# Kernel tuning notes

Measured on AMD Instinct MI355X. Metric: run time of the kernel, lower is better.

Reference implementation:

```python
import jax, jax.numpy as jnp
import numpy as np

BIN_SIZE = 128
DIST_MULT = 0.1
CLIP_LOW = 0.0
LN_EPS = 1e-6


def setup_inputs() -> dict:
    key = jax.random.key(0)
    ks = jax.random.split(key, 16)
    B, N, F, DD, MAXB = 8, 12800, 256, 128, 200
    s = 0.05  # ~TF random_normal initializer stddev
    inp = {}
    inp["x"] = jax.random.normal(ks[0], (B, N, F), jnp.float32)
    inp["msk"] = jax.random.uniform(ks[1], (B, N)) < 0.9
    # layernorm params
    inp["ln_g"] = jnp.ones((F,), jnp.float32)
    inp["ln_b"] = jnp.zeros((F,), jnp.float32)
    # ffn_dist: Dense(DD, elu) -> Dense(DD)
    inp["w1"] = jax.random.normal(ks[2], (F, DD), jnp.float32) * s
    inp["b1"] = jax.random.normal(ks[3], (DD,), jnp.float32) * s
    inp["w2"] = jax.random.normal(ks[4], (DD, DD), jnp.float32) * s
    inp["b2"] = jax.random.normal(ks[5], (DD,), jnp.float32) * s
    # LSH random rotations (non-trainable)
    inp["rot"] = jax.random.normal(ks[6], (DD, MAXB // 2), jnp.float32) * s
    # two GHConvDense layers (hidden=F -> output=F)
    inp["theta0"] = jax.random.normal(ks[7], (F, F), jnp.float32) * s
    inp["wh0"] = jax.random.normal(ks[8], (F, F), jnp.float32) * s
    inp["wt0"] = jax.random.normal(ks[9], (F, F), jnp.float32) * s
    inp["bt0"] = jax.random.normal(ks[10], (F,), jnp.float32) * s
    inp["theta1"] = jax.random.normal(ks[11], (F, F), jnp.float32) * s
    inp["wh1"] = jax.random.normal(ks[12], (F, F), jnp.float32) * s
    inp["wt1"] = jax.random.normal(ks[13], (F, F), jnp.float32) * s
    inp["bt1"] = jax.random.normal(ks[14], (F,), jnp.float32) * s
    return inp


def _ghconv(x, adj, mskf, theta, wh, wt, bt):
    # x: [B,nb,bs,F], adj: [B,nb,bs,bs], mskf: [B,nb,bs,1]
    deg = jnp.clip(jnp.sum(jnp.abs(adj), axis=-1), 0.0, 1000.0)  # [B,nb,bs]
    norm = ((deg + 1e-6) ** -0.5)[..., None] * mskf
    f_hom = jnp.matmul(x * mskf, theta) * mskf
    f_hom = jnp.matmul(adj, f_hom * norm) * norm
    f_het = jnp.matmul(x * mskf, wh)
    gate = jax.nn.sigmoid(jnp.matmul(x, wt) + bt)
    out = gate * f_hom + (1.0 - gate) * f_het
    return jax.nn.elu(out) * mskf


def _forward(x, msk, ln_g, ln_b, w1, b1, w2, b2, rot,
             theta0, wh0, wt0, bt0, theta1, wh1, wt1, bt1):
    B, N, F = x.shape
    nbins = N // BIN_SIZE
    # layernorm
    mu = jnp.mean(x, axis=-1, keepdims=True)
    var = jnp.mean((x - mu) ** 2, axis=-1, keepdims=True)
    xn = (x - mu) * jax.lax.rsqrt(var + LN_EPS) * ln_g + ln_b
    # ffn_dist
    xd = jnp.matmul(jax.nn.elu(jnp.matmul(xn, w1) + b1), w2) + b2  # [B,N,DD]
    # LSH binning
    mul = jnp.matmul(xd, rot[:, : nbins // 2])
    cmul = jnp.concatenate([mul, -mul], axis=-1)  # [B,N,nbins]
    bin_idx = jnp.argmax(cmul, axis=-1) + jnp.where(~msk, nbins - 1, 0)
    bins_split = jnp.argsort(bin_idx, axis=-1).reshape(B, nbins, BIN_SIZE)
    flat = bins_split.reshape(B, N)
    # gather into bins
    xd_b = jnp.take_along_axis(xd, flat[:, :, None], axis=1).reshape(B, nbins, BIN_SIZE, -1)
    x_b = jnp.take_along_axis(xn, flat[:, :, None], axis=1).reshape(B, nbins, BIN_SIZE, F)
    mskf = msk.astype(x.dtype)[:, :, None]
    m_b = jnp.take_along_axis(mskf, flat[:, :, None], axis=1).reshape(B, nbins, BIN_SIZE, 1)
    # pairwise gaussian kernel within bins
    na = jnp.sum(xd_b * xd_b, axis=-1)
    D2 = na[..., :, None] - 2.0 * jnp.einsum("bnie,bnje->bnij", xd_b, xd_b) + na[..., None, :]
    dm = jnp.exp(-DIST_MULT * jnp.sqrt(jnp.maximum(D2, 1e-6)))
    dm = jnp.clip(dm, CLIP_LOW, 1.0)
    m = m_b[..., 0]
    dm = dm * m[:, :, :, None] * m[:, :, None, :]
    # graph convs
    x_b = _ghconv(x_b, dm, m_b, theta0, wh0, wt0, bt0)
    x_b = _ghconv(x_b, dm, m_b, theta1, wh1, wt1, bt1)
    # reverse LSH scatter
    pts = x_b.reshape(B, N, F)
    x_enc = jnp.zeros((B, N, F), pts.dtype).at[jnp.arange(B)[:, None], flat].set(pts)
    return x_enc


def reference(x, msk, ln_g, ln_b, w1, b1, w2, b2, rot,
              theta0, wh0, wt0, bt0, theta1, wh1, wt1, bt1):
    return _forward(x, msk, ln_g, ln_b, w1, b1, w2, b2, rot,
                    theta0, wh0, wt0, bt0, theta1, wh1, wt1, bt1)
```

## Files before the change

kernel.cpp:

```cpp
#include <hip/hip_runtime.h>
#include <math.h>

#define BB 8
#define NN 12800
#define FF 256
#define DDIM 128
#define NBINS 100
#define BSIZE 128
#define NROT 50
#define NIDS 199
#define PTS (BB*NN)

#define OFF_OUT0 ((size_t)157286400)
#define OFF_DMB  ((size_t)209715200)
#define OFF_WB   ((size_t)235929600)
#define OFF_NORM ((size_t)236716032)
#define OFF_MF   ((size_t)237125632)
#define OFF_BIN  ((size_t)237535232)
#define OFF_FLAT ((size_t)237944832)
#define OFF_MSKI ((size_t)238354432)
#define OFF_HIST ((size_t)238764032)
#define OFF_OFFS ((size_t)239400832)
#define OFF_FLAG ((size_t)240037632)
#define OFF_CNT  ((size_t)240037696)
#define OFF_LIST ((size_t)240037760)
#define OFF_W1H  ((size_t)240447360)
#define OFF_W1L  ((size_t)240512896)
#define OFF_W2H  ((size_t)240578432)
#define OFF_W2L  ((size_t)240611200)
#define OFF_RH   ((size_t)240643968)
#define OFF_RL   ((size_t)240660352)
#define HISTBYTES (8*100*199*4)

using short8  = __attribute__((ext_vector_type(8))) short;
using floatx4 = __attribute__((ext_vector_type(4))) float;

__device__ __forceinline__ ushort f2b(float f) {
    unsigned u = __float_as_uint(f);
    unsigned r = (u + 0x7FFFu + ((u >> 16) & 1u)) >> 16;
    return (ushort)r;
}
__device__ __forceinline__ float b2f(ushort h) {
    return __uint_as_float(((unsigned)h) << 16);
}
__device__ __forceinline__ uint4 pack8(const ushort* o) {
    uint4 u;
    u.x = (unsigned)o[0] | ((unsigned)o[1] << 16);
    u.y = (unsigned)o[2] | ((unsigned)o[3] << 16);
    u.z = (unsigned)o[4] | ((unsigned)o[5] << 16);
    u.w = (unsigned)o[6] | ((unsigned)o[7] << 16);
    return u;
}

__global__ void k_maskflag(const int* mi, int* flag) {
    __shared__ int notInt, notFloat;
    if (threadIdx.x == 0) { notInt = 0; notFloat = 0; }
    __syncthreads();
    int v = mi[threadIdx.x];
    if (v != 0 && v != 1) atomicOr(&notInt, 1);
    if (v != 0 && v != 0x3F800000) atomicOr(&notFloat, 1);
    __syncthreads();
    if (threadIdx.x == 0) flag[0] = (!notInt) ? 0 : ((!notFloat) ? 2 : 1);
}

__global__ void k_masknorm(const void* msk, const int* flag, int* mski) {
    int i = blockIdx.x * blockDim.x + threadIdx.x;
    if (i >= PTS) return;
    int f = flag[0];
    int v;
    if (f == 0)      v = ((const int*)msk)[i] != 0;
    else if (f == 2) v = ((const float*)msk)[i] != 0.0f;
    else             v = ((const unsigned char*)msk)[i] != 0;
    mski[i] = v;
}

__global__ __launch_bounds__(256) void k_wprep(
    const float* s0, const float* s1, const float* s2,
    const float* s3, const float* s4, const float* s5,
    ushort* d0, ushort* d1, ushort* d2, ushort* d3, ushort* d4, ushort* d5)
{
    __shared__ float Ls[64 * 65];
    const float* src; ushort* dst;
    switch (blockIdx.y) {
        case 0: src = s0; dst = d0; break;
        case 1: src = s1; dst = d1; break;
        case 2: src = s2; dst = d2; break;
        case 3: src = s3; dst = d3; break;
        case 4: src = s4; dst = d4; break;
        default: src = s5; dst = d5; break;
    }
    int t = blockIdx.x;
    int kb = (t & 3) * 64, nb = (t >> 2) * 64;
    int tid = threadIdx.x;
    for (int q = 0; q < 4; ++q) {
        int g = q * 256 + tid;
        int kl = g >> 4, f4 = g & 15;
        float4 v = *(const float4*)(src + (size_t)(kb + kl) * 256 + nb + f4 * 4);
        Ls[kl * 65 + f4 * 4 + 0] = v.x;
        Ls[kl * 65 + f4 * 4 + 1] = v.y;
        Ls[kl * 65 + f4 * 4 + 2] = v.z;
        Ls[kl * 65 + f4 * 4 + 3] = v.w;
    }
    __syncthreads();
    for (int q = 0; q < 2; ++q) {
        int g = q * 256 + tid;
        int nl = g >> 3, wg = g & 7;
        ushort o[8];
        #pragma unroll
        for (int c = 0; c < 8; ++c) o[c] = f2b(Ls[(wg * 8 + c) * 65 + nl]);
        *(uint4*)(dst + (size_t)(nb + nl) * 256 + kb + wg * 8) = pack8(o);
    }
}

__global__ __launch_bounds__(256) void k_wsplit(const float* __restrict__ src, int K, int N,
                                               int srcN, int nvalid,
                                               ushort* __restrict__ dh, ushort* __restrict__ dl) {
    __shared__ float Ls[64 * 65];
    int tilesN = N >> 6;
    int kb = (blockIdx.x / tilesN) * 64, nb = (blockIdx.x % tilesN) * 64;
    int tid = threadIdx.x;
    for (int q = 0; q < 4; ++q) {
        int g = q * 256 + tid;
        int kl = g >> 4, c4 = (g & 15) * 4;
        #pragma unroll
        for (int j = 0; j < 4; ++j) {
            int n = nb + c4 + j;
            float v = (n < nvalid) ? src[(size_t)(kb + kl) * srcN + n] : 0.f;
            Ls[kl * 65 + c4 + j] = v;
        }
    }
    __syncthreads();
    for (int q = 0; q < 2; ++q) {
        int g = q * 256 + tid;
        int nl = g >> 3, wg = g & 7;
        ushort oh[8], ol[8];
        #pragma unroll
        for (int c = 0; c < 8; ++c) {
            float v = Ls[(wg * 8 + c) * 65 + nl];
            ushort h = f2b(v);
            oh[c] = h;
            ol[c] = f2b(v - b2f(h));
        }
        *(uint4*)(dh + (size_t)(nb + nl) * K + kb + wg * 8) = pack8(oh);
        *(uint4*)(dl + (size_t)(nb + nl) * K + kb + wg * 8) = pack8(ol);
    }
}

__device__ __forceinline__ void stage_async(const ushort* __restrict__ src, size_t pitch,
                                            const int* __restrict__ rowmap, int rowbase, size_t kbase,
                                            ushort* lds, int nrows, int tid) {
    int lane = tid & 63, wid = tid >> 6;
    int total = nrows * 8;
    for (int b0 = 0; b0 < total; b0 += 512) {
        int g = b0 + wid * 64 + lane;
        int row = g >> 3;
        int ck = (g & 7) ^ (row & 7);
        size_t srow = rowmap ? (size_t)rowmap[rowbase + row] : (size_t)(rowbase + row);
        const ushort* gp = src + srow * pitch + kbase + ck * 8;
        ushort* lp = lds + (size_t)(b0 + wid * 64) * 8;
        __builtin_amdgcn_global_load_lds(
            (const __attribute__((address_space(1))) unsigned int*)gp,
            (__attribute__((address_space(3))) unsigned int*)lp, 16, 0, 0);
    }
}

__device__ __forceinline__ short8 frag_ld(const ushort* lds, int row, int kc, int lane) {
    int w0 = (kc * 16 + ((lane >> 4) << 2)) ^ ((row & 7) << 2);
    return *(const short8*)((const char*)lds + row * 128 + w0 * 4);
}

__global__ __launch_bounds__(512, 4) void k_stage1(
    const float* __restrict__ x, const float* __restrict__ g, const float* __restrict__ be,
    const float* __restrict__ b1, const float* __restrict__ b2,
    const ushort* __restrict__ w1h, const ushort* __restrict__ w1l,
    const ushort* __restrict__ w2h, const ushort* __restrict__ w2l,
    const ushort* __restrict__ rth, const ushort* __restrict__ rtl,
    const int* __restrict__ mski,
    ushort* __restrict__ xn_out, ushort* __restrict__ xdh_out, ushort* __restrict__ xdl_out,
    int* __restrict__ bin_out, int* __restrict__ fixlist, int* __restrict__ fixcnt)
{
    __shared__ ushort lXh[4 * 2048];
    __shared__ ushort lXl[4 * 2048];
    __shared__ ushort lWh[8192];
    __shared__ ushort lWl[8192];
    int tid = threadIdx.x, lane = tid & 63, wid = tid >> 6;
    int base = blockIdx.x * 32;
    int l15 = lane & 15;
    int r4 = (lane >> 4) * 4;

    stage_async(w1h, 256, nullptr, 0, 0, lWh, 128, tid);
    stage_async(w1l, 256, nullptr, 0, 0, lWl, 128, tid);

    {
        int row = tid >> 4, sub = tid & 15;
        const float* xr = x + (size_t)(base + row) * FF + sub * 16;
        float v[16];
        float s = 0.f;
        #pragma unroll
        for (int q = 0; q < 4; ++q) {
            float4 f = *(const float4*)(xr + q * 4);
            v[q*4+0] = f.x; v[q*4+1] = f.y; v[q*4+2] = f.z; v[q*4+3] = f.w;
            s += f.x + f.y + f.z + f.w;
        }
        s += __shfl_xor(s, 1, 16); s += __shfl_xor(s, 2, 16);
        s += __shfl_xor(s, 4, 16); s += __shfl_xor(s, 8, 16);
        float mu = s * (1.f / 256.f);
        float s2 = 0.f;
        #pragma unroll
        for (int q = 0; q < 16; ++q) { float d = v[q] - mu; s2 += d * d; }
        s2 += __shfl_xor(s2, 1, 16); s2 += __shfl_xor(s2, 2, 16);
        s2 += __shfl_xor(s2, 4, 16); s2 += __shfl_xor(s2, 8, 16);
        float rs = 1.0f / sqrtf(s2 * (1.f / 256.f) + 1e-6f);
        ushort* xo = xn_out + (size_t)(base + row) * FF + sub * 16;
        #pragma unroll
        for (int j = 0; j < 2; ++j) {
            int i0 = sub * 16 + j * 8;
            float4 g0 = *(const float4*)(g + i0);
            float4 g1 = *(const float4*)(g + i0 + 4);
            float4 e0 = *(const float4*)(be + i0);
            float4 e1 = *(const float4*)(be + i0 + 4);
            float gv[8] = {g0.x,g0.y,g0.z,g0.w,g1.x,g1.y,g1.z,g1.w};
            float ev[8] = {e0.x,e0.y,e0.z,e0.w,e1.x,e1.y,e1.z,e1.w};
            ushort hh[8], ll[8];
            #pragma unroll
            for (int c = 0; c < 8; ++c) {
                float xv = (v[j*8+c] - mu) * rs * gv[c] + ev[c];
                ushort h = f2b(xv);
                hh[c] = h;
                ll[c] = f2b(xv - b2f(h));
            }
            uint4 uh = pack8(hh), ul = pack8(ll);
            *(uint4*)(xo + j * 8) = uh;
            int kb = i0 >> 6;
            int wg = (i0 & 63) >> 3;
            int w0 = (wg * 4) ^ ((row & 7) << 2);
            *(uint4*)((char*)lXh + kb * 4096 + row * 128 + w0 * 4) = uh;
            *(uint4*)((char*)lXl + kb * 4096 + row * 128 + w0 * 4) = ul;
        }
    }
    __syncthreads();

    int mg = wid >> 2, ng = wid & 3;
    int wm = mg * 16, wn = ng * 32;
    floatx4 zf = {0.f, 0.f, 0.f, 0.f};

    floatx4 acc[2];
    acc[0] = zf; acc[1] = zf;
    for (int kb = 0; kb < 4; ++kb) {
        #pragma unroll
        for (int kc = 0; kc < 2; ++kc) {
            short8 ah, al, bh[2], bl[2];
            ah = frag_ld(lXh + kb * 2048, wm + l15, kc, lane);
            al = frag_ld(lXl + kb * 2048, wm + l15, kc, lane);
            #pragma unroll
            for (int n = 0; n < 2; n++) {
                bh[n] = frag_ld(lWh, wn + n * 16 + l15, kc, lane);
                bl[n] = frag_ld(lWl, wn + n * 16 + l15, kc, lane);
            }
            #pragma unroll
            for (int n = 0; n < 2; n++) {
                acc[n] = __builtin_amdgcn_mfma_f32_16x16x32_bf16(ah, bh[n], acc[n], 0, 0, 0);
                acc[n] = __builtin_amdgcn_mfma_f32_16x16x32_bf16(ah, bl[n], acc[n], 0, 0, 0);
                acc[n] = __builtin_amdgcn_mfma_f32_16x16x32_bf16(al, bh[n], acc[n], 0, 0, 0);
            }
        }
        __syncthreads();
        if (kb < 3) {
            stage_async(w1h, 256, nullptr, 0, (size_t)(kb + 1) * 64, lWh, 128, tid);
            stage_async(w1l, 256, nullptr, 0, (size_t)(kb + 1) * 64, lWl, 128, tid);
            __syncthreads();
        }
    }
    stage_async(w2h, 128, nullptr, 0, 0, lWh, 128, tid);
    stage_async(w2l, 128, nullptr, 0, 0, lWl, 128, tid);
    {
        #pragma unroll
        for (int n = 0; n < 2; n++) {
            int cg = wn + n * 16 + l15;
            float b1v = b1[cg];
            int slab = cg >> 6, c64 = cg & 63;
            int wg = c64 >> 3, e = c64 & 7;
            #pragma unroll
            for (int i = 0; i < 4; i++) {
                int r = wm + r4 + i;
                float hv = acc[n][i] + b1v;
                hv = (hv > 0.f) ? hv : expm1f(hv);
                ushort h = f2b(hv);
                int w0 = (wg * 4) ^ ((r & 7) << 2);
                int idx = slab * 2048 + r * 64 + w0 * 2 + e;
                lXh[idx] = h;
                lXl[idx] = f2b(hv - b2f(h));
            }
        }
    }
    __syncthreads();

    floatx4 acc2[2];
    acc2[0] = zf; acc2[1] = zf;
    for (int kb = 0; kb < 2; ++kb) {
        #pragma unroll
        for (int kc = 0; kc < 2; ++kc) {
            short8 ah, al, bh[2], bl[2];
            ah = frag_ld(lXh + kb * 2048, wm + l15, kc, lane);
            al = frag_ld(lXl + kb * 2048, wm + l15, kc, lane);
            #pragma unroll
            for (int n = 0; n < 2; n++) {
                bh[n] = frag_ld(lWh, wn + n * 16 + l15, kc, lane);
                bl[n] = frag_ld(lWl, wn + n * 16 + l15, kc, lane);
            }
            #pragma unroll
            for (int n = 0; n < 2; n++) {
                acc2[n] = __builtin_amdgcn_mfma_f32_16x16x32_bf16(ah, bh[n], acc2[n], 0, 0, 0);
                acc2[n] = __builtin_amdgcn_mfma_f32_16x16x32_bf16(ah, bl[n], acc2[n], 0, 0, 0);
                acc2[n] = __builtin_amdgcn_mfma_f32_16x16x32_bf16(al, bh[n], acc2[n], 0, 0, 0);
            }
        }
        __syncthreads();
        if (kb == 0) {
            stage_async(w2h, 128, nullptr, 0, 64, lWh, 128, tid);
            stage_async(w2l, 128, nullptr, 0, 64, lWl, 128, tid);
            __syncthreads();
        }
    }
    stage_async(rth, 128, nullptr, 0, 0, lWh, 64, tid);
    stage_async(rtl, 128, nullptr, 0, 0, lWl, 64, tid);
    stage_async(rth, 128, nullptr, 0, 64, lWh + 4096, 64, tid);
    stage_async(rtl, 128, nullptr, 0, 64, lWl + 4096, 64, tid);
    {
        #pragma unroll
        for (int n = 0; n < 2; n++) {
            int cg = wn + n * 16 + l15;
            float b2v = b2[cg];
            int slab = 2 + (cg >> 6), c64 = cg & 63;
            int wg = c64 >> 3, e = c64 & 7;
            #pragma unroll
            for (int i = 0; i < 4; i++) {
                int r = wm + r4 + i;
                float xv = acc2[n][i] + b2v;
                ushort h = f2b(xv);
                ushort lo = f2b(xv - b2f(h));
                size_t go = (size_t)(base + r) * DDIM + cg;
                xdh_out[go] = h;
                xdl_out[go] = lo;
                int w0 = (wg * 4) ^ ((r & 7) << 2);
                int idx = slab * 2048 + r * 64 + w0 * 2 + e;
                lXh[idx] = h;
                lXl[idx] = lo;
            }
        }
    }
    __syncthreads();

    floatx4 acc3 = zf;
    int wn3 = ng * 16;
    for (int kb = 0; kb < 2; ++kb) {
        #pragma unroll
        for (int kc = 0; kc < 2; ++kc) {
            short8 ah, al, bh, bl;
            ah = frag_ld(lXh + (2 + kb) * 2048, wm + l15, kc, lane);
            al = frag_ld(lXl + (2 + kb) * 2048, wm + l15, kc, lane);
            bh = frag_ld(lWh + kb * 4096, wn3 + l15, kc, lane);
            bl = frag_ld(lWl + kb * 4096, wn3 + l15, kc, lane);
            acc3 = __builtin_amdgcn_mfma_f32_16x16x32_bf16(ah, bh, acc3, 0, 0, 0);
            acc3 = __builtin_amdgcn_mfma_f32_16x16x32_bf16(ah, bl, acc3, 0, 0, 0);
            acc3 = __builtin_amdgcn_mfma_f32_16x16x32_bf16(al, bh, acc3, 0, 0, 0);
        }
    }
    __syncthreads();
    float* lMul = (float*)lXh;
    {
        #pragma unroll
        for (int i = 0; i < 4; i++) {
            int r = wm + r4 + i;
            lMul[r * 65 + wn3 + l15] = acc3[i];
        }
    }
    __syncthreads();

    {
        int p = tid >> 4, q = tid & 15;
        float v1 = -1e30f, v2 = -1e30f; int i1 = 1 << 29;
        #pragma unroll
        for (int j = 0; j < 4; ++j) {
            int c = q * 4 + j;
            if (c < 50) {
                float m = lMul[p * 65 + c];
                float wv, lv; int wi, li;
                if (m >= 0.f) { wv = m; wi = c; lv = -m; li = 50 + c; }
                else          { wv = -m; wi = 50 + c; lv = m; li = c; }
                if (wv > v1 || (wv == v1 && wi < i1)) { v2 = v1; v1 = wv; i1 = wi; }
                else if (wv > v2) v2 = wv;
                if (lv > v1 || (lv == v1 && li < i1)) { v2 = v1; v1 = lv; i1 = li; }
                else if (lv > v2) v2 = lv;
            }
        }
        #pragma unroll
        for (int off = 1; off < 16; off <<= 1) {
            float o1 = __shfl_xor(v1, off, 16);
            int   oi = __shfl_xor(i1, off, 16);
            float o2 = __shfl_xor(v2, off, 16);
            bool take = (o1 > v1) || (o1 == v1 && oi < i1);
            float small = take ? v1 : o1;
            if (take) { v1 = o1; i1 = oi; }
            v2 = fmaxf(fmaxf(v2, o2), small);
        }
        if (q == 0) {
            int pt = base + p;
            bin_out[pt] = i1 + (mski[pt] ? 0 : (NBINS - 1));
            float tau = 3e-4f + 1.5e-3f * v1;
            if (v1 - v2 < tau) {
                int pos = atomicAdd(fixcnt, 1);
                fixlist[pos] = pt;
            }
        }
    }
}

__global__ __launch_bounds__(64) void k_fixup(
    const float* __restrict__ x, const float* __restrict__ g, const float* __restrict__ be,
    const float* __restrict__ w1, const float* __restrict__ b1,
    const float* __restrict__ w2, const float* __restrict__ b2,
    const float* __restrict__ rot, const int* __restrict__ mski,
    const int* __restrict__ fixlist, const int* __restrict__ fixcnt,
    int* __restrict__ bin_out)
{
    __shared__ double xn_s[256];
    __shared__ double h_s[128];
    __shared__ double xd_s[128];
    int lane = threadIdx.x;
    int n = fixcnt[0];
    for (int e = blockIdx.x; e < n; e += gridDim.x) {
        int pt = fixlist[e];
        const float* xr = x + (size_t)pt * FF;
        double s = 0.0, xv[4];
        #pragma unroll
        for (int q = 0; q < 4; q++) { xv[q] = (double)xr[lane + q * 64]; s += xv[q]; }
        #pragma unroll
        for (int off = 1; off < 64; off <<= 1) s += __shfl_xor(s, off, 64);
        double mu = s * (1.0 / 256.0);
        double s2 = 0.0;
        #pragma unroll
        for (int q = 0; q < 4; q++) { double d = xv[q] - mu; s2 += d * d; }
        #pragma unroll
        for (int off = 1; off < 64; off <<= 1) s2 += __shfl_xor(s2, off, 64);
        double rs = 1.0 / sqrt(s2 * (1.0 / 256.0) + 1e-6);
        #pragma unroll
        for (int q = 0; q < 4; q++) {
            int i = lane + q * 64;
            xn_s[i] = (xv[q] - mu) * rs * (double)g[i] + (double)be[i];
        }
        __syncthreads();
        #pragma unroll
        for (int q = 0; q < 2; q++) {
            int j = lane + q * 64;
            double a0 = 0.0, a1 = 0.0;
            for (int k = 0; k < FF; k += 2) {
                a0 += xn_s[k] * (double)w1[k * DDIM + j];
                a1 += xn_s[k + 1] * (double)w1[(k + 1) * DDIM + j];
            }
            double a = (double)b1[j] + a0 + a1;
            h_s[j] = (a > 0.0) ? a : expm1(a);
        }
        __syncthreads();
        #pragma unroll
        for (int q = 0; q < 2; q++) {
            int j = lane + q * 64;
            double a0 = 0.0, a1 = 0.0;
            for (int k = 0; k < DDIM; k += 2) {
                a0 += h_s[k] * (double)w2[k * DDIM + j];
                a1 += h_s[k + 1] * (double)w2[(k + 1) * DDIM + j];
            }
            xd_s[j] = (double)b2[j] + a0 + a1;
        }
        __syncthreads();
        double v; int idx;
        if (lane < NROT) {
            double m = 0.0;
            for (int k = 0; k < DDIM; k++) m += xd_s[k] * (double)rot[k * 100 + lane];
            if (m >= 0.0) { v = m; idx = lane; } else { v = -m; idx = 50 + lane; }
        } else { v = -1e300; idx = 1 << 29; }
        #pragma unroll
        for (int off = 1; off < 64; off <<= 1) {
            double ov = __shfl_xor(v, off, 64);
            int oi = __shfl_xor(idx, off, 64);
            if (ov > v || (ov == v && oi < idx)) { v = ov; idx = oi; }
        }
        if (lane == 0) bin_out[pt] = idx + (mski[pt] ? 0 : (NBINS - 1));
        __syncthreads();
    }
}

__global__ void k_count(const int* __restrict__ bin, int* __restrict__ hist) {
    int c = blockIdx.x % 100, b = blockIdx.x / 100;
    int t = threadIdx.x;
    int v = bin[b * NN + c * BSIZE + t];
    atomicAdd(&hist[(b * 100 + c) * NIDS + v], 1);
}

__global__ void k_offsets(const int* __restrict__ hist, int* __restrict__ offs) {
    __shared__ int tot[NIDS];
    __shared__ int start[NIDS];
    int b = blockIdx.x, v = threadIdx.x;
    if (v < NIDS) {
        int s = 0;
        for (int c = 0; c < 100; c++) s += hist[(b * 100 + c) * NIDS + v];
        tot[v] = s;
    }
    __syncthreads();
    if (threadIdx.x == 0) {
        int run = 0;
        for (int i = 0; i < NIDS; i++) { start[i] = run; run += tot[i]; }
    }
    __syncthreads();
    if (v < NIDS) {
        int run = start[v];
        for (int c = 0; c < 100; c++) {
            offs[(b * 100 + c) * NIDS + v] = run;
            run += hist[(b * 100 + c) * NIDS + v];
        }
    }
}

__global__ void k_scatter(const int* __restrict__ bin, const int* __restrict__ offs,
                          const int* __restrict__ mski, int* __restrict__ flat,
                          float* __restrict__ mf) {
    __shared__ int sv[BSIZE];
    int c = blockIdx.x % 100, b = blockIdx.x / 100;
    int t = threadIdx.x;
    int n = c * BSIZE + t;
    int v = bin[b * NN + n];
    sv[t] = v;
    __syncthreads();
    int rank = 0;
    for (int u = 0; u < t; u++) rank += (sv[u] == v);
    int r = offs[(b * 100 + c) * NIDS + v] + rank;
    flat[b * NN + r] = b * NN + n;
    mf[b * NN + r] = mski[b * NN + n] ? 1.0f : 0.0f;
}

__global__ __launch_bounds__(512, 4) void k_dm(const ushort* __restrict__ xdh, const ushort* __restrict__ xdl,
                                               const int* __restrict__ flat, const float* __restrict__ mf,
                                               ushort* __restrict__ dmb, float* __restrict__ norm) {
    __shared__ ushort lX[32768];
    __shared__ float na[128];
    __shared__ float ml[128];
    __shared__ float ps[512];
    int tid = threadIdx.x, lane = tid & 63, wid = tid >> 6;
    int g = blockIdx.x;
    int rowbase = g * 128;
    int l15 = lane & 15;
    int r4 = (lane >> 4) * 4;
    int mg = wid >> 2, ng = wid & 3;
    int wm = mg * 64, wn = ng * 32;
    floatx4 zf = {0.f, 0.f, 0.f, 0.f};

    stage_async(xdh, 128, flat, rowbase, 0, lX, 128, tid);
    stage_async(xdh, 128, flat, rowbase, 64, lX + 8192, 128, tid);
    stage_async(xdl, 128, flat, rowbase, 0, lX + 16384, 128, tid);
    stage_async(xdl, 128, flat, rowbase, 64, lX + 24576, 128, tid);
    if (tid < 128) ml[tid] = mf[rowbase + tid];
    __syncthreads();

    {
        int row = tid >> 2, part = tid & 3;
        float s = 0.f;
        #pragma unroll
        for (int kb = 0; kb < 2; ++kb) {
            const ushort* ph = lX + kb * 8192 + row * 64 + part * 16;
            #pragma unroll
            for (int q = 0; q < 2; ++q) {
                uint4 uh = *(const uint4*)(ph + q * 8);
                uint4 ul = *(const uint4*)(ph + 16384 + q * 8);
                const unsigned* wh_ = (const unsigned*)&uh;
                const unsigned* wl_ = (const unsigned*)&ul;
                #pragma unroll
                for (int w = 0; w < 4; ++w) {
                    float x0 = b2f((ushort)(wh_[w] & 0xFFFFu)) + b2f((ushort)(wl_[w] & 0xFFFFu));
                    float x1 = b2f((ushort)(wh_[w] >> 16)) + b2f((ushort)(wl_[w] >> 16));
                    s = fmaf(x0, x0, s);
                    s = fmaf(x1, x1, s);
                }
            }
        }
        s += __shfl_xor(s, 1, 4);
        s += __shfl_xor(s, 2, 4);
        if (part == 0) na[row] = s;
    }

    floatx4 acc[4][2];
    #pragma unroll
    for (int m = 0; m < 4; m++) { acc[m][0] = zf; acc[m][1] = zf; }
    for (int kb = 0; kb < 2; ++kb) {
        #pragma unroll
        for (int kc = 0; kc < 2; ++kc) {
            short8 ah[4], al[4], bh[2], bl[2];
            #pragma unroll
            for (int m = 0; m < 4; m++) {
                ah[m] = frag_ld(lX + kb * 8192, wm + m * 16 + l15, kc, lane);
                al[m] = frag_ld(lX + 16384 + kb * 8192, wm + m * 16 + l15, kc, lane);
            }
            #pragma unroll
            for (int n = 0; n < 2; n++) {
                bh[n] = frag_ld(lX + kb * 8192, wn + n * 16 + l15, kc, lane);
                bl[n] = frag_ld(lX + 16384 + kb * 8192, wn + n * 16 + l15, kc, lane);
            }
            #pragma unroll
            for (int m = 0; m < 4; m++)
                #pragma unroll
                for (int n = 0; n < 2; n++) {
                    acc[m][n] = __builtin_amdgcn_mfma_f32_16x16x32_bf16(ah[m], bh[n], acc[m][n], 0, 0, 0);
                    acc[m][n] = __builtin_amdgcn_mfma_f32_16x16x32_bf16(ah[m], bl[n], acc[m][n], 0, 0, 0);
                    acc[m][n] = __builtin_amdgcn_mfma_f32_16x16x32_bf16(al[m], bh[n], acc[m][n], 0, 0, 0);
                }
        }
    }
    __syncthreads();

    ushort* Ls = lX;
    for (int m = 0; m < 4; ++m) {
        int r0 = wm + m * 16 + r4;
        float rs[4] = {0.f, 0.f, 0.f, 0.f};
        #pragma unroll
        for (int n = 0; n < 2; ++n) {
            int c = wn + n * 16 + l15;
            float nac = na[c], mlc = ml[c];
            #pragma unroll
            for (int i = 0; i < 4; ++i) {
                int r = r0 + i;
                float D2 = na[r] - 2.f * acc[m][n][i] + nac;
                float dv = expf(-0.1f * sqrtf(fmaxf(D2, 1e-6f)));
                dv *= ml[r] * mlc;
                rs[i] += dv;
                Ls[r * 136 + c] = f2b(dv);
            }
        }
        #pragma unroll
        for (int off = 1; off < 16; off <<= 1) {
            #pragma unroll
            for (int i = 0; i < 4; ++i) rs[i] += __shfl_xor(rs[i], off, 16);
        }
        if (l15 == 0) {
            #pragma unroll
            for (int i = 0; i < 4; ++i) ps[(r0 + i) * 4 + ng] = rs[i];
        }
    }
    __syncthreads();

    #pragma unroll
    for (int it = 0; it < 4; ++it) {
        int gi = it * 512 + tid;
        int row = gi >> 4, ch = gi & 15;
        uint4 v = *(const uint4*)(Ls + row * 136 + ch * 8);
        *(uint4*)(dmb + (size_t)g * 16384 + row * 128 + ch * 8) = v;
    }
    if (tid < 128) {
        float deg = ps[tid * 4 + 0] + ps[tid * 4 + 1] + ps[tid * 4 + 2] + ps[tid * 4 + 3];
        deg = fminf(deg, 1000.0f);
        norm[rowbase + tid] = (1.0f / sqrtf(deg + 1e-6f)) * ml[tid];
    }
}

template<int LAYER>
__global__ __launch_bounds__(512, 4) void k_layer(
    const ushort* __restrict__ A, const int* __restrict__ rowmap,
    const ushort* __restrict__ ThT, const ushort* __restrict__ WhT, const ushort* __restrict__ WtT,
    const float* __restrict__ bt, const ushort* __restrict__ dmb,
    const float* __restrict__ norm, const float* __restrict__ mf,
    ushort* __restrict__ outb, float* __restrict__ outf, const int* __restrict__ flatscat)
{
    __shared__ char smem[81920];
    ushort* lAbuf = (ushort*)smem;
    ushort* lB    = (ushort*)(smem + 32768);
    ushort* lT    = (ushort*)smem;
    ushort* ldm   = (ushort*)(smem + 32768);

    int tid = threadIdx.x, lane = tid & 63, wid = tid >> 6;
    int bid = blockIdx.x;
    int grp = bid >> 5, within = bid & 31;
    int nh = within >> 3, g = grp * 8 + (within & 7);
    int rowbase = g * 128, nbase = nh * 64;
    int l15 = lane & 15;
    int r4 = (lane >> 4) * 4;
    int wm = (wid >> 1) * 32, wn = (wid & 1) * 32;
    const ushort* dmg = dmb + (size_t)g * 16384;
    floatx4 zf = {0.f, 0.f, 0.f, 0.f};

    stage_async(A, 256, rowmap, rowbase, 0, lAbuf, 128, tid);
    stage_async(ThT, 256, nullptr, nbase, 0, lB + 0 * 4096, 64, tid);
    stage_async(WhT, 256, nullptr, nbase, 0, lB + 2 * 4096, 64, tid);
    stage_async(WtT, 256, nullptr, nbase, 0, lB + 4 * 4096, 64, tid);
    __syncthreads();

    floatx4 accT[2][2], accH[2][2], accG[2][2];
    #pragma unroll
    for (int m = 0; m < 2; m++)
        #pragma unroll
        for (int n = 0; n < 2; n++) { accT[m][n] = zf; accH[m][n] = zf; accG[m][n] = zf; }
    for (int kb = 0; kb < 4; ++kb) {
        if (kb < 3) {
            int pp = (kb + 1) & 1;
            stage_async(A, 256, rowmap, rowbase, (size_t)(kb + 1) * 64, lAbuf + pp * 8192, 128, tid);
            stage_async(ThT, 256, nullptr, nbase, (size_t)(kb + 1) * 64, lB + (0 + pp) * 4096, 64, tid);
            stage_async(WhT, 256, nullptr, nbase, (size_t)(kb + 1) * 64, lB + (2 + pp) * 4096, 64, tid);
            stage_async(WtT, 256, nullptr, nbase, (size_t)(kb + 1) * 64, lB + (4 + pp) * 4096, 64, tid);
        }
        const ushort* lA = lAbuf + (kb & 1) * 8192;
        const ushort* sTh = lB + (0 + (kb & 1)) * 4096;
        const ushort* sWh = lB + (2 + (kb & 1)) * 4096;
        const ushort* sWt = lB + (4 + (kb & 1)) * 4096;
        #pragma unroll
        for (int kc = 0; kc < 2; ++kc) {
            short8 a[2], bt_[2], bh_[2], bg_[2];
            #pragma unroll
            for (int m = 0; m < 2; m++) a[m] = frag_ld(lA, wm + m * 16 + l15, kc, lane);
            #pragma unroll
            for (int n = 0; n < 2; n++) {
                bt_[n] = frag_ld(sTh, wn + n * 16 + l15, kc, lane);
                bh_[n] = frag_ld(sWh, wn + n * 16 + l15, kc, lane);
                bg_[n] = frag_ld(sWt, wn + n * 16 + l15, kc, lane);
            }
            #pragma unroll
            for (int m = 0; m < 2; m++)
                #pragma unroll
                for (int n = 0; n < 2; n++) {
                    accT[m][n] = __builtin_amdgcn_mfma_f32_16x16x32_bf16(a[m], bt_[n], accT[m][n], 0, 0, 0);
                    accH[m][n] = __builtin_amdgcn_mfma_f32_16x16x32_bf16(a[m], bh_[n], accH[m][n], 0, 0, 0);
                    accG[m][n] = __builtin_amdgcn_mfma_f32_16x16x32_bf16(a[m], bg_[n], accG[m][n], 0, 0, 0);
                }
        }
        __syncthreads();
    }

    stage_async(dmg, 128, nullptr, 0, 0, ldm, 128, tid);
    stage_async(dmg, 128, nullptr, 0, 64, ldm + 8192, 128, tid);

    {
        #pragma unroll
        for (int m = 0; m < 2; m++) {
            float4 nv = *(const float4*)(norm + rowbase + wm + m * 16 + r4);
            float nvv[4] = {nv.x, nv.y, nv.z, nv.w};
            int jloc0 = wm + m * 16 + r4;
            int jb = jloc0 >> 6, jj = jloc0 & 63;
            #pragma unroll
            for (int n = 0; n < 2; n++) {
                int cloc = wn + n * 16 + l15;
                char* bp = (char*)(lT + jb * 4096) + cloc * 128;
                int cx = (cloc & 7) << 2;
                ushort t0 = f2b(accT[m][n][0] * nvv[0]);
                ushort t1 = f2b(accT[m][n][1] * nvv[1]);
                ushort t2 = f2b(accT[m][n][2] * nvv[2]);
                ushort t3 = f2b(accT[m][n][3] * nvv[3]);
                *(unsigned*)(bp + ((((jj >> 1) + 0) ^ cx) << 2)) = (unsigned)t0 | ((unsigned)t1 << 16);
                *(unsigned*)(bp + ((((jj >> 1) + 1) ^ cx) << 2)) = (unsigned)t2 | ((unsigned)t3 << 16);
            }
        }
    }
    __syncthreads();

    floatx4 accFH[2][2];
    #pragma unroll
    for (int m = 0; m < 2; m++) { accFH[m][0] = zf; accFH[m][1] = zf; }
    for (int kb = 0; kb < 2; ++kb) {
        #pragma unroll
        for (int kc = 0; kc < 2; ++kc) {
            short8 a[2], b[2];
            #pragma unroll
            for (int m = 0; m < 2; m++) a[m] = frag_ld(ldm + kb * 8192, wm + m * 16 + l15, kc, lane);
            #pragma unroll
            for (int n = 0; n < 2; n++) b[n] = frag_ld(lT + kb * 4096, wn + n * 16 + l15, kc, lane);
            #pragma unroll
            for (int m = 0; m < 2; m++)
                #pragma unroll
                for (int n = 0; n < 2; n++)
                    accFH[m][n] = __builtin_amdgcn_mfma_f32_16x16x32_bf16(a[m], b[n], accFH[m][n], 0, 0, 0);
        }
    }
    __syncthreads();

    for (int m = 0; m < 2; m++) {
        int r0l = wm + m * 16 + r4;
        int r0g = rowbase + r0l;
        float4 mv = *(const float4*)(mf + r0g);
        float4 nv = *(const float4*)(norm + r0g);
        float mvv[4] = {mv.x, mv.y, mv.z, mv.w};
        float nvv[4] = {nv.x, nv.y, nv.z, nv.w};
        float vals[2][4];
        #pragma unroll
        for (int n = 0; n < 2; n++) {
            int cg = nbase + wn + n * 16 + l15;
            float btc = bt[cg];
            #pragma unroll
            for (int i = 0; i < 4; i++) {
                float gate = 1.f / (1.f + expf(-(accG[m][n][i] + btc)));
                float fh = accFH[m][n][i] * nvv[i];
                float het = mvv[i] * accH[m][n][i];
                float o = gate * fh + (1.f - gate) * het;
                o = (o > 0.f) ? o : expm1f(o);
                vals[n][i] = o * mvv[i];
            }
        }
        if (LAYER == 0) {
            ushort* Ls = (ushort*)smem;
            int bbase = wid * 512;
            #pragma unroll
            for (int n = 0; n < 2; n++)
                #pragma unroll
                for (int i = 0; i < 4; i++)
                    Ls[bbase + (r4 + i) * 32 + n * 16 + l15] = f2b(vals[n][i]);
            __builtin_amdgcn_s_waitcnt(0);
            #pragma unroll
            for (int it = 0; it < 2; ++it) {
                int lr = (lane >> 3) + it * 8;
                int lc4 = (lane & 7) * 4;
                ushort4 tv = *(const ushort4*)(Ls + bbase + lr * 32 + lc4);
                int rg = rowbase + wm + m * 16 + lr;
                *(ushort4*)(outb + (size_t)rg * 256 + nbase + wn + lc4) = tv;
            }
        } else {
            float* Ls = (float*)smem;
            int bbase = wid * 512;
            #pragma unroll
            for (int n = 0; n < 2; n++)
                #pragma unroll
                for (int i = 0; i < 4; i++)
                    Ls[bbase + (r4 + i) * 32 + n * 16 + l15] = vals[n][i];
            __builtin_amdgcn_s_waitcnt(0);
            #pragma unroll
            for (int it = 0; it < 2; ++it) {
                int lr = (lane >> 3) + it * 8;
                int lc4 = (lane & 7) * 4;
                float4 tv = *(const float4*)(Ls + bbase + lr * 32 + lc4);
                int rg = rowbase + wm + m * 16 + lr;
                int dst = flatscat[rg];
                *(float4*)(outf + (size_t)dst * 256 + nbase + wn + lc4) = tv;
            }
        }
    }
}

extern "C" void kernel_launch(void* const* d_in, const int* in_sizes, int n_in,
                              void* d_out, int out_size, void* d_ws, size_t ws_size,
                              hipStream_t stream) {
    const float* x    = (const float*)d_in[0];
    const void*  msk  = d_in[1];
    const float* ln_g = (const float*)d_in[2];
    const float* ln_b = (const float*)d_in[3];
    const float* w1   = (const float*)d_in[4];
    const float* b1   = (const float*)d_in[5];
    const float* w2   = (const float*)d_in[6];
    const float* b2   = (const float*)d_in[7];
    const float* rot  = (const float*)d_in[8];
    const float* th0  = (const float*)d_in[9];
    const float* wh0  = (const float*)d_in[10];
    const float* wt0  = (const float*)d_in[11];
    const float* bt0  = (const float*)d_in[12];
    const float* th1  = (const float*)d_in[13];
    const float* wh1  = (const float*)d_in[14];
    const float* wt1  = (const float*)d_in[15];
    const float* bt1  = (const float*)d_in[16];

    char* ws = (char*)d_ws;
    ushort* out0 = (ushort*)(ws + OFF_OUT0);
    ushort* dmb  = (ushort*)(ws + OFF_DMB);
    ushort* wb   = (ushort*)(ws + OFF_WB);
    ushort* wbth0 = wb + 0 * 65536;
    ushort* wbwh0 = wb + 1 * 65536;
    ushort* wbwt0 = wb + 2 * 65536;
    ushort* wbth1 = wb + 3 * 65536;
    ushort* wbwh1 = wb + 4 * 65536;
    ushort* wbwt1 = wb + 5 * 65536;
    float* norm = (float*)(ws + OFF_NORM);
    float* mf   = (float*)(ws + OFF_MF);
    int*   bin  = (int*)(ws + OFF_BIN);
    int*   flat = (int*)(ws + OFF_FLAT);
    int*   mski = (int*)(ws + OFF_MSKI);
    int*   hist = (int*)(ws + OFF_HIST);
    int*   offs = (int*)(ws + OFF_OFFS);
    int*   flag = (int*)(ws + OFF_FLAG);
    int*   fixcnt = (int*)(ws + OFF_CNT);
    int*   fixlist = (int*)(ws + OFF_LIST);
    ushort* w1h = (ushort*)(ws + OFF_W1H);
    ushort* w1l = (ushort*)(ws + OFF_W1L);
    ushort* w2h = (ushort*)(ws + OFF_W2H);
    ushort* w2l = (ushort*)(ws + OFF_W2L);
    ushort* rth = (ushort*)(ws + OFF_RH);
    ushort* rtl = (ushort*)(ws + OFF_RL);
    ushort* xdh = (ushort*)d_out;
    ushort* xdl = xdh + (size_t)PTS * DDIM;
    ushort* xnb = (ushort*)((char*)d_out + (size_t)PTS * DDIM * 4);

    hipMemsetAsync(hist, 0, HISTBYTES, stream);
    hipMemsetAsync(fixcnt, 0, 4, stream);
    k_maskflag<<<1, 256, 0, stream>>>((const int*)msk, flag);
    k_masknorm<<<PTS / 256, 256, 0, stream>>>(msk, flag, mski);
    k_wprep<<<dim3(16, 6), 256, 0, stream>>>(th0, wh0, wt0, th1, wh1, wt1,
                                             wbth0, wbwh0, wbwt0, wbth1, wbwh1, wbwt1);
    k_wsplit<<<8, 256, 0, stream>>>(w1, 256, 128, 128, 128, w1h, w1l);
    k_wsplit<<<4, 256, 0, stream>>>(w2, 128, 128, 128, 128, w2h, w2l);
    k_wsplit<<<2, 256, 0, stream>>>(rot, 128, 64, 100, 50, rth, rtl);
    k_stage1<<<PTS / 32, 512, 0, stream>>>(x, ln_g, ln_b, b1, b2,
                                           w1h, w1l, w2h, w2l, rth, rtl, mski,
                                           xnb, xdh, xdl, bin, fixlist, fixcnt);
    k_fixup<<<4096, 64, 0, stream>>>(x, ln_g, ln_b, w1, b1, w2, b2, rot, mski,
                                     fixlist, fixcnt, bin);
    k_count<<<800, 128, 0, stream>>>(bin, hist);
    k_offsets<<<8, 256, 0, stream>>>(hist, offs);
    k_scatter<<<800, 128, 0, stream>>>(bin, offs, mski, flat, mf);
    k_dm<<<800, 512, 0, stream>>>(xdh, xdl, flat, mf, dmb, norm);
    k_layer<0><<<3200, 512, 0, stream>>>(xnb, flat, wbth0, wbwh0, wbwt0, bt0,
                                         dmb, norm, mf, out0, nullptr, nullptr);
    k_layer<1><<<3200, 512, 0, stream>>>(out0, nullptr, wbth1, wbwh1, wbwt1, bt1,
                                         dmb, norm, mf, nullptr, (float*)d_out, flat);
}
```

Baseline: 389.7 us.

## Read stage1 weight fragments directly from global memory, drop LDS weight staging

Removes the LDS buffers for the w1, w2 and rotation weights in k_stage1. B-fragments are now loaded straight from global memory (relying on L2/L1 caching) instead of being staged asynchronously into LDS, which also removes the per-k-block barriers. The launch bound rises from 4 to 8 blocks per CU, since LDS use per block drops by half. In exchange every wave issues redundant global loads of the weights, and the lower register budget may add latency or spills.

```diff
diff --git a/kernel.cpp b/kernel.cpp
--- a/kernel.cpp
+++ b/kernel.cpp
@@ -169,7 +169,12 @@
     return *(const short8*)((const char*)lds + row * 128 + w0 * 4);
 }
 
-__global__ __launch_bounds__(512, 4) void k_stage1(
+__device__ __forceinline__ short8 bfrag_g(const ushort* __restrict__ W, int Kpitch,
+                                          int row, int k0) {
+    return *(const short8*)(W + (size_t)row * Kpitch + k0);
+}
+
+__global__ __launch_bounds__(512, 8) void k_stage1(
     const float* __restrict__ x, const float* __restrict__ g, const float* __restrict__ be,
     const float* __restrict__ b1, const float* __restrict__ b2,
     const ushort* __restrict__ w1h, const ushort* __restrict__ w1l,
@@ -181,15 +186,11 @@
 {
     __shared__ ushort lXh[4 * 2048];
     __shared__ ushort lXl[4 * 2048];
-    __shared__ ushort lWh[8192];
-    __shared__ ushort lWl[8192];
     int tid = threadIdx.x, lane = tid & 63, wid = tid >> 6;
     int base = blockIdx.x * 32;
     int l15 = lane & 15;
     int r4 = (lane >> 4) * 4;
-
-    stage_async(w1h, 256, nullptr, 0, 0, lWh, 128, tid);
-    stage_async(w1l, 256, nullptr, 0, 0, lWl, 128, tid);
+    int kf = (lane >> 4) * 8;
 
     {
         int row = tid >> 4, sub = tid & 15;
@@ -249,30 +250,21 @@
     for (int kb = 0; kb < 4; ++kb) {
         #pragma unroll
         for (int kc = 0; kc < 2; ++kc) {
-            short8 ah, al, bh[2], bl[2];
-            ah = frag_ld(lXh + kb * 2048, wm + l15, kc, lane);
-            al = frag_ld(lXl + kb * 2048, wm + l15, kc, lane);
+            int k0 = kb * 64 + kc * 32 + kf;
+            short8 ah = frag_ld(lXh + kb * 2048, wm + l15, kc, lane);
+            short8 al = frag_ld(lXl + kb * 2048, wm + l15, kc, lane);
             #pragma unroll
             for (int n = 0; n < 2; n++) {
-                bh[n] = frag_ld(lWh, wn + n * 16 + l15, kc, lane);
-                bl[n] = frag_ld(lWl, wn + n * 16 + l15, kc, lane);
-            }
-            #pragma unroll
-            for (int n = 0; n < 2; n++) {
-                acc[n] = __builtin_amdgcn_mfma_f32_16x16x32_bf16(ah, bh[n], acc[n], 0, 0, 0);
-                acc[n] = __builtin_amdgcn_mfma_f32_16x16x32_bf16(ah, bl[n], acc[n], 0, 0, 0);
-                acc[n] = __builtin_amdgcn_mfma_f32_16x16x32_bf16(al, bh[n], acc[n], 0, 0, 0);
-            }
-        }
-        __syncthreads();
-        if (kb < 3) {
-            stage_async(w1h, 256, nullptr, 0, (size_t)(kb + 1) * 64, lWh, 128, tid);
-            stage_async(w1l, 256, nullptr, 0, (size_t)(kb + 1) * 64, lWl, 128, tid);
-            __syncthreads();
-        }
-    }
-    stage_async(w2h, 128, nullptr, 0, 0, lWh, 128, tid);
-    stage_async(w2l, 128, nullptr, 0, 0, lWl, 128, tid);
+                int rowb = wn + n * 16 + l15;
+                short8 bh = bfrag_g(w1h, 256, rowb, k0);
+                short8 bl = bfrag_g(w1l, 256, rowb, k0);
+                acc[n] = __builtin_amdgcn_mfma_f32_16x16x32_bf16(ah, bh, acc[n], 0, 0, 0);
+                acc[n] = __builtin_amdgcn_mfma_f32_16x16x32_bf16(ah, bl, acc[n], 0, 0, 0);
+                acc[n] = __builtin_amdgcn_mfma_f32_16x16x32_bf16(al, bh, acc[n], 0, 0, 0);
+            }
+        }
+    }
+    __syncthreads();
     {
         #pragma unroll
         for (int n = 0; n < 2; n++) {
@@ -300,32 +292,21 @@
     for (int kb = 0; kb < 2; ++kb) {
         #pragma unroll
         for (int kc = 0; kc < 2; ++kc) {
-            short8 ah, al, bh[2], bl[2];
-            ah = frag_ld(lXh + kb * 2048, wm + l15, kc, lane);
-            al = frag_ld(lXl + kb * 2048, wm + l15, kc, lane);
+            int k0 = kb * 64 + kc * 32 + kf;
+            short8 ah = frag_ld(lXh + kb * 2048, wm + l15, kc, lane);
+            short8 al = frag_ld(lXl + kb * 2048, wm + l15, kc, lane);
             #pragma unroll
             for (int n = 0; n < 2; n++) {
-                bh[n] = frag_ld(lWh, wn + n * 16 + l15, kc, lane);
-                bl[n] = frag_ld(lWl, wn + n * 16 + l15, kc, lane);
-            }
-            #pragma unroll
-            for (int n = 0; n < 2; n++) {
-                acc2[n] = __builtin_amdgcn_mfma_f32_16x16x32_bf16(ah, bh[n], acc2[n], 0, 0, 0);
-                acc2[n] = __builtin_amdgcn_mfma_f32_16x16x32_bf16(ah, bl[n], acc2[n], 0, 0, 0);
-                acc2[n] = __builtin_amdgcn_mfma_f32_16x16x32_bf16(al, bh[n], acc2[n], 0, 0, 0);
-            }
-        }
-        __syncthreads();
-        if (kb == 0) {
-            stage_async(w2h, 128, nullptr, 0, 64, lWh, 128, tid);
-            stage_async(w2l, 128, nullptr, 0, 64, lWl, 128, tid);
-            __syncthreads();
-        }
-    }
-    stage_async(rth, 128, nullptr, 0, 0, lWh, 64, tid);
-    stage_async(rtl, 128, nullptr, 0, 0, lWl, 64, tid);
-    stage_async(rth, 128, nullptr, 0, 64, lWh + 4096, 64, tid);
-    stage_async(rtl, 128, nullptr, 0, 64, lWl + 4096, 64, tid);
+                int rowb = wn + n * 16 + l15;
+                short8 bh = bfrag_g(w2h, 128, rowb, k0);
+                short8 bl = bfrag_g(w2l, 128, rowb, k0);
+                acc2[n] = __builtin_amdgcn_mfma_f32_16x16x32_bf16(ah, bh, acc2[n], 0, 0, 0);
+                acc2[n] = __builtin_amdgcn_mfma_f32_16x16x32_bf16(ah, bl, acc2[n], 0, 0, 0);
+                acc2[n] = __builtin_amdgcn_mfma_f32_16x16x32_bf16(al, bh, acc2[n], 0, 0, 0);
+            }
+        }
+    }
+    __syncthreads();
     {
         #pragma unroll
         for (int n = 0; n < 2; n++) {
@@ -356,11 +337,12 @@
     for (int kb = 0; kb < 2; ++kb) {
         #pragma unroll
         for (int kc = 0; kc < 2; ++kc) {
-            short8 ah, al, bh, bl;
-            ah = frag_ld(lXh + (2 + kb) * 2048, wm + l15, kc, lane);
-            al = frag_ld(lXl + (2 + kb) * 2048, wm + l15, kc, lane);
-            bh = frag_ld(lWh + kb * 4096, wn3 + l15, kc, lane);
-            bl = frag_ld(lWl + kb * 4096, wn3 + l15, kc, lane);
+            int k0 = kb * 64 + kc * 32 + kf;
+            short8 ah = frag_ld(lXh + (2 + kb) * 2048, wm + l15, kc, lane);
+            short8 al = frag_ld(lXl + (2 + kb) * 2048, wm + l15, kc, lane);
+            int rowb = wn3 + l15;
+            short8 bh = bfrag_g(rth, 128, rowb, k0);
+            short8 bl = bfrag_g(rtl, 128, rowb, k0);
             acc3 = __builtin_amdgcn_mfma_f32_16x16x32_bf16(ah, bh, acc3, 0, 0, 0);
             acc3 = __builtin_amdgcn_mfma_f32_16x16x32_bf16(ah, bl, acc3, 0, 0, 0);
             acc3 = __builtin_amdgcn_mfma_f32_16x16x32_bf16(al, bh, acc3, 0, 0, 0);
```

Result: slower. 496.9 us (+27.5%).
